# Kernel tuning notes

Measured on AMD Instinct MI355X. Metric: run time of the kernel, lower is better.

Reference implementation:

```python
import jax, jax.numpy as jnp
import numpy as np

TEMPERATURE = 0.07
HARD_K = 10
N, D, NUM_CLASSES = 8192, 256, 128


def setup_inputs() -> dict:
    key = jax.random.key(0)
    kf, kl = jax.random.split(key)
    feats = jax.random.normal(kf, (N, D), dtype=jnp.float32)
    labels = jax.random.randint(kl, (N,), 0, NUM_CLASSES, dtype=jnp.int64)
    return {"feats": feats, "labels": labels}


def _loss(feats, labels):
    n = feats.shape[0]
    # F.normalize(dim=-1) with eps=1e-12
    norm = jnp.maximum(jnp.linalg.norm(feats, axis=-1, keepdims=True), 1e-12)
    z = feats / norm
    sim = (z @ z.T) / TEMPERATURE  # [N, N]

    same = labels[:, None] == labels[None, :]
    eye = jnp.eye(n, dtype=bool)
    same_ns = same & ~eye          # same label, excluding self
    diff = ~same                   # different label

    neg_inf = jnp.float32(-jnp.inf)
    # uniform random positive per row via Gumbel-max over the same-label mask
    g = jax.random.gumbel(jax.random.key(42), (n, n), dtype=jnp.float32)
    pos_idx = jnp.argmax(jnp.where(same_ns, g, neg_inf), axis=1)  # [N]
    pos_logit = jnp.take_along_axis(sim, pos_idx[:, None], axis=1)[:, 0]

    # hard negatives: top-k of sims over different-label columns
    neg_sims = jnp.where(diff, sim, neg_inf)
    hard_vals, _ = jax.lax.top_k(neg_sims, HARD_K)  # [N, K]; exp(-inf)=0 handles rows with <K negatives

    num = jnp.exp(pos_logit)
    den = num + jnp.sum(jnp.exp(hard_vals), axis=1)
    li = -jnp.log(jnp.maximum(num / jnp.maximum(den, 1e-8), 1e-8))

    valid = jnp.any(same_ns, axis=1) & jnp.any(diff, axis=1)
    cnt = jnp.maximum(jnp.sum(valid), 1)
    return jnp.sum(jnp.where(valid, li, 0.0)) / cnt.astype(li.dtype)


def reference(feats, labels):
    return _loss(feats, labels)
```

## Files before the change

kernel.cpp:

```cpp
#include <hip/hip_runtime.h>
#include <cstdint>
#include <math.h>

#define N_     8192
#define D_     256
#define NLBL   128
#define TEMP_INV 14.285714285714286f
#define HARDK  10
#define THETA  0.16f
#define GCAP   256

#define RB     256
#define NCHUNK 32
#define CHUNK  (N_ / NCHUNK)
#define TILES  (CHUNK / 32)
#define CSLOT  16

typedef __attribute__((ext_vector_type(8)))  short bf16x8;
typedef __attribute__((ext_vector_type(16))) float f32x16;

__device__ __forceinline__ uint32_t rotl32(uint32_t x, int n) {
  return (x << n) | (x >> (32 - n));
}
__device__ uint32_t tf_bits(uint32_t idx) {
  uint32_t x0 = 0u, x1 = idx;
  const uint32_t k0 = 0u, k1 = 42u;
  const uint32_t k2 = k0 ^ k1 ^ 0x1BD11BDAu;
  x0 += k0; x1 += k1;
#define TFR(r) { x0 += x1; x1 = rotl32(x1, r); x1 ^= x0; }
  TFR(13) TFR(15) TFR(26) TFR(6)
  x0 += k1; x1 += k2 + 1u;
  TFR(17) TFR(29) TFR(16) TFR(24)
  x0 += k2; x1 += k0 + 2u;
  TFR(13) TFR(15) TFR(26) TFR(6)
  x0 += k0; x1 += k1 + 3u;
  TFR(17) TFR(29) TFR(16) TFR(24)
  x0 += k1; x1 += k2 + 4u;
  TFR(13) TFR(15) TFR(26) TFR(6)
  x0 += k2; x1 += k0 + 5u;
#undef TFR
  return x0 ^ x1;
}

__device__ __forceinline__ unsigned short f2bf(float x) {
  uint32_t b = __float_as_uint(x);
  return (unsigned short)((b + 0x7FFFu + ((b >> 16) & 1u)) >> 16);
}

__global__ __launch_bounds__(256) void prep_kernel(const float* __restrict__ feats,
                                                   float* __restrict__ inv_norm,
                                                   unsigned short* __restrict__ zbf) {
  const int i = blockIdx.x * 4 + (threadIdx.x >> 6);
  const int l = threadIdx.x & 63;
  float4 v = ((const float4*)feats)[(size_t)i * 64 + l];
  float ss = v.x * v.x + v.y * v.y + v.z * v.z + v.w * v.w;
#pragma unroll
  for (int o = 32; o; o >>= 1) ss += __shfl_xor(ss, o);
  float inv = 1.0f / fmaxf(sqrtf(ss), 1e-12f);
  if (l == 0) inv_norm[i] = inv;
  uint2 p;
  p.x = (uint32_t)f2bf(v.x * inv) | ((uint32_t)f2bf(v.y * inv) << 16);
  p.y = (uint32_t)f2bf(v.z * inv) | ((uint32_t)f2bf(v.w * inv) << 16);
  ((uint2*)zbf)[(size_t)i * 64 + l] = p;
}

__global__ __launch_bounds__(256) void transpose_kernel(const unsigned short* __restrict__ zbf,
                                                        unsigned short* __restrict__ zt) {
  __shared__ uint4 tile[64][33];
  const int tid = threadIdx.x;
  const int row0 = blockIdx.x * 64;
#pragma unroll
  for (int it = 0; it < 8; ++it) {
    int idx = it * 256 + tid;
    int r = idx >> 5, c = idx & 31;
    tile[r][c] = ((const uint4*)zbf)[(size_t)(row0 + r) * 32 + c];
  }
  __syncthreads();
#pragma unroll
  for (int it = 0; it < 8; ++it) {
    int c = it * 4 + (tid >> 6);
    int r = tid & 63;
    ((uint4*)zt)[(size_t)c * N_ + row0 + r] = tile[r][c];
  }
}

__global__ __launch_bounds__(256) void group_kernel(const int* __restrict__ labels,
                                                    uint32_t* __restrict__ mask_g,
                                                    int* __restrict__ glist,
                                                    int* __restrict__ cnt_g) {
  const int b = blockIdx.x;
  const int tid = threadIdx.x, lane = tid & 63, wv = tid >> 6;
  __shared__ int lcnt;
  if (tid == 0) lcnt = 0;
  __syncthreads();
  for (int it = 0; it < N_; it += 256) {
    int col = it + tid;
    bool pred = (labels[col] == b);
    unsigned long long m = __ballot(pred);
    if (lane == 0) {
      int w0 = (it + wv * 64) >> 5;
      mask_g[b * 256 + w0]     = (uint32_t)m;
      mask_g[b * 256 + w0 + 1] = (uint32_t)(m >> 32);
    }
    if (pred) {
      int p = atomicAdd(&lcnt, 1);
      if (p < GCAP) glist[b * GCAP + p] = col;
    }
  }
  __syncthreads();
  if (tid == 0) cnt_g[b] = lcnt;
}

__device__ __forceinline__ void stage_tile(const unsigned short* zt, char (*AbK)[1024],
                                           int colT, int wid, int l, int kg) {
  const char* base = (const char*)zt + ((size_t)kg * N_ + colT + (l & 31)) * 16;
#pragma unroll
  for (int q = 0; q < 4; ++q) {
    const int kk = wid * 4 + q;
    __builtin_amdgcn_global_load_lds(
        (const __attribute__((address_space(1))) void*)(base + (size_t)kk * (2 * N_ * 16)),
        (__attribute__((address_space(3))) void*)(&AbK[kk][0]), 16, 0, 0);
  }
}

#define INS8(H0,H1,H2,H3,H4,H5,H6,H7,POS,C) \
  { H0 = (POS==0)?(C):H0; H1 = (POS==1)?(C):H1; H2 = (POS==2)?(C):H2; H3 = (POS==3)?(C):H3; \
    H4 = (POS==4)?(C):H4; H5 = (POS==5)?(C):H5; H6 = (POS==6)?(C):H6; H7 = (POS==7)?(C):H7; \
    ++POS; }

__global__ __launch_bounds__(256, 2) void collect_kernel(const unsigned short* __restrict__ zt,
                                                         const int* __restrict__ labels,
                                                         const uint32_t* __restrict__ mask_g,
                                                         float* __restrict__ vals,
                                                         int* __restrict__ counts) {
  __shared__ char Ab[3][16][1024];

  const int tid = threadIdx.x;
  const int l = tid & 63, wid = tid >> 6;
  const int kg = l >> 5;
  const int bx = blockIdx.x;
  const int rc = bx & 31, cc = bx >> 5;
  const int row0 = rc * RB;
  const int col0 = cc * CHUNK;
  const int rowA = row0 + wid * 64 + (l & 31);
  const int rowB = rowA + 32;
  const int labA = labels[rowA];
  const int labB = labels[rowB];

  uint32_t mA[TILES], mB[TILES];
  {
    const uint4* ma = (const uint4*)(mask_g + labA * 256 + (col0 >> 5));
    const uint4* mb = (const uint4*)(mask_g + labB * 256 + (col0 >> 5));
    uint4 a0 = ma[0], a1 = ma[1], b0 = mb[0], b1 = mb[1];
    mA[0]=a0.x; mA[1]=a0.y; mA[2]=a0.z; mA[3]=a0.w;
    mA[4]=a1.x; mA[5]=a1.y; mA[6]=a1.z; mA[7]=a1.w;
    mB[0]=b0.x; mB[1]=b0.y; mB[2]=b0.z; mB[3]=b0.w;
    mB[4]=b1.x; mB[5]=b1.y; mB[6]=b1.z; mB[7]=b1.w;
  }

  bf16x8 bfA[16], bfB[16];
  {
    const uint4* ztq = (const uint4*)zt;
#pragma unroll
    for (int kk = 0; kk < 16; ++kk) {
      bfA[kk] = *(const bf16x8*)&ztq[(size_t)(kk * 2 + kg) * N_ + rowA];
      bfB[kk] = *(const bf16x8*)&ztq[(size_t)(kk * 2 + kg) * N_ + rowB];
    }
  }

  float hA0=0,hA1=0,hA2=0,hA3=0,hA4=0,hA5=0,hA6=0,hA7=0;
  float hB0=0,hB1=0,hB2=0,hB3=0,hB4=0,hB5=0,hB6=0,hB7=0;
  int posA = 0, posB = 0;

  stage_tile(zt, Ab[0], col0 + 0 * 32, wid, l, kg);
  stage_tile(zt, Ab[1], col0 + 1 * 32, wid, l, kg);
  asm volatile("s_waitcnt vmcnt(4)" ::: "memory");
  __builtin_amdgcn_s_barrier();
  __builtin_amdgcn_sched_barrier(0);

#pragma unroll
  for (int t = 0; t < TILES; ++t) {
    if (t + 2 < TILES) stage_tile(zt, Ab[(t + 2) % 3], col0 + (t + 2) * 32, wid, l, kg);

    const uint32_t wshA = mA[t] >> (kg * 4);
    const uint32_t wshB = mB[t] >> (kg * 4);

    f32x16 accA, accB;
#pragma unroll
    for (int r = 0; r < 16; ++r) { accA[r] = 0.f; accB[r] = 0.f; }
    __builtin_amdgcn_s_setprio(1);
#pragma unroll
    for (int kk = 0; kk < 16; ++kk) {
      bf16x8 a = *(const bf16x8*)&Ab[t % 3][kk][l * 16];
      accA = __builtin_amdgcn_mfma_f32_32x32x16_bf16(a, bfA[kk], accA, 0, 0, 0);
      accB = __builtin_amdgcn_mfma_f32_32x32x16_bf16(a, bfB[kk], accB, 0, 0, 0);
    }
    __builtin_amdgcn_s_setprio(0);

#pragma unroll
    for (int r = 0; r < 16; ++r) {
      const int cpos = (r & 3) + 8 * (r >> 2);
      float cA = accA[r];
      if ((((wshA >> cpos) & 1u) == 0u) && (cA > THETA)) {
        INS8(hA0,hA1,hA2,hA3,hA4,hA5,hA6,hA7, posA, cA);
      }
      float cB = accB[r];
      if ((((wshB >> cpos) & 1u) == 0u) && (cB > THETA)) {
        INS8(hB0,hB1,hB2,hB3,hB4,hB5,hB6,hB7, posB, cB);
      }
    }

    if (t < TILES - 2) {
      asm volatile("s_waitcnt vmcnt(4)" ::: "memory");
      __builtin_amdgcn_s_barrier();
      __builtin_amdgcn_sched_barrier(0);
    } else if (t == TILES - 2) {
      asm volatile("s_waitcnt vmcnt(0)" ::: "memory");
      __builtin_amdgcn_s_barrier();
      __builtin_amdgcn_sched_barrier(0);
    }
  }

  {
    float4 a0 = {hA0, hA1, hA2, hA3};
    float4 a1 = {hA4, hA5, hA6, hA7};
    float4 b0 = {hB0, hB1, hB2, hB3};
    float4 b1 = {hB4, hB5, hB6, hB7};
    float* dA = vals + ((size_t)rowA * NCHUNK + cc) * CSLOT + kg * 8;
    float* dB = vals + ((size_t)rowB * NCHUNK + cc) * CSLOT + kg * 8;
    *(float4*)(dA)     = a0;
    *(float4*)(dA + 4) = a1;
    *(float4*)(dB)     = b0;
    *(float4*)(dB + 4) = b1;
    counts[(rowA * NCHUNK + cc) * 2 + kg] = posA;
    counts[(rowB * NCHUNK + cc) * 2 + kg] = posB;
  }
}

__global__ __launch_bounds__(256) void finalize_kernel(
    const float* __restrict__ feats, const int* __restrict__ labels,
    const float* __restrict__ inv_norm,
    const int* __restrict__ glist, const int* __restrict__ cnt_g,
    const int* __restrict__ counts, const float* __restrict__ vals,
    float* __restrict__ li, int* __restrict__ valid) {
  const int row = blockIdx.x * 4 + (threadIdx.x >> 6);
  const int lane = threadIdx.x & 63;
  const int lab = labels[row];
  const int gc = cnt_g[lab];
  const int gn = gc < GCAP ? gc : GCAP;
  const float4* feats4 = (const float4*)feats;

  uint32_t bk = 0u; int bj = -1;
  for (int e = lane; e < gn; e += 64) {
    int j = glist[lab * GCAP + e];
    if (j != row) {
      uint32_t key = tf_bits((uint32_t)row * (uint32_t)N_ + (uint32_t)j) >> 9;
      if (bj < 0 || key > bk || (key == bk && j < bj)) { bk = key; bj = j; }
    }
  }
#pragma unroll
  for (int o = 32; o; o >>= 1) {
    uint32_t ok = __shfl_xor(bk, o);
    int oj = __shfl_xor(bj, o);
    if (oj >= 0 && (bj < 0 || ok > bk || (ok == bk && oj < bj))) { bk = ok; bj = oj; }
  }

  float pc = 0.f;
  if (bj >= 0) {
    float4 a = feats4[(size_t)row * 64 + lane];
    float4 b = feats4[(size_t)bj * 64 + lane];
    float p = a.x * b.x + a.y * b.y + a.z * b.z + a.w * b.w;
#pragma unroll
    for (int o = 32; o; o >>= 1) p += __shfl_xor(p, o);
    pc = p * inv_norm[row] * inv_norm[bj];
  }

  float vv[8];
  int ovf = 0;
#pragma unroll
  for (int q = 0; q < 8; ++q) {
    int s = lane + 64 * q;
    int cell = s >> 4, wi = s & 15;
    int c0 = counts[(row * NCHUNK + cell) * 2 + 0];
    int c1 = counts[(row * NCHUNK + cell) * 2 + 1];
    ovf |= ((c0 > 8) || (c1 > 8)) ? 1 : 0;
    float val = vals[(size_t)row * (NCHUNK * CSLOT) + s];
    bool live = (wi < 8) ? (wi < c0) : ((wi - 8) < c1);
    vv[q] = live ? val : -INFINITY;
  }

  float num = expf(pc * TEMP_INV);
  float den = num;
  int got = 0;
#pragma unroll 1
  for (int it = 0; it < HARDK; ++it) {
    float lm = fmaxf(fmaxf(fmaxf(vv[0], vv[1]), fmaxf(vv[2], vv[3])),
                     fmaxf(fmaxf(vv[4], vv[5]), fmaxf(vv[6], vv[7])));
    float wm = lm;
#pragma unroll
    for (int o = 32; o; o >>= 1) wm = fmaxf(wm, __shfl_xor(wm, o));
    if (wm < -1e37f) break;
    den += expf(wm * TEMP_INV);
    ++got;
    unsigned long long b = __ballot(lm == wm);
    int fl = __ffsll((long long)b) - 1;
    if (lane == fl) {
      if      (vv[0] == wm) vv[0] = -INFINITY;
      else if (vv[1] == wm) vv[1] = -INFINITY;
      else if (vv[2] == wm) vv[2] = -INFINITY;
      else if (vv[3] == wm) vv[3] = -INFINITY;
      else if (vv[4] == wm) vv[4] = -INFINITY;
      else if (vv[5] == wm) vv[5] = -INFINITY;
      else if (vv[6] == wm) vv[6] = -INFINITY;
      else                  vv[7] = -INFINITY;
    }
  }

  const int ndiff = N_ - gc;
  const bool vld = (bj >= 0) && (ndiff > 0);
  const int want = ndiff < HARDK ? ndiff : HARDK;

  if (vld && (__any(ovf) || got < want)) {
    float tk[HARDK];
#pragma unroll
    for (int k = 0; k < HARDK; ++k) tk[k] = -INFINITY;
    const float invr = inv_norm[row];
    const float4 a = feats4[(size_t)row * 64 + lane];
#pragma unroll 1
    for (int j = 0; j < N_; ++j) {
      if (j == row || labels[j] == lab) continue;
      float4 b = feats4[(size_t)j * 64 + lane];
      float p = a.x * b.x + a.y * b.y + a.z * b.z + a.w * b.w;
#pragma unroll
      for (int o = 32; o; o >>= 1) p += __shfl_xor(p, o);
      float c = p * invr * inv_norm[j];
      if (c > tk[0]) {
        tk[0] = c;
#pragma unroll
        for (int q = 0; q < HARDK - 1; ++q)
          if (tk[q] > tk[q + 1]) { float tmp = tk[q]; tk[q] = tk[q + 1]; tk[q + 1] = tmp; }
      }
    }
    den = num;
#pragma unroll
    for (int k = 0; k < HARDK; ++k)
      if (tk[k] > -1e37f) den += expf(tk[k] * TEMP_INV);
  }

  float L = 0.f;
  if (vld) L = -logf(fmaxf(num / fmaxf(den, 1e-8f), 1e-8f));
  if (lane == 0) {
    li[row] = L;
    valid[row] = vld ? 1 : 0;
  }
}

__global__ __launch_bounds__(256) void reduce_kernel(const float* __restrict__ li,
                                                     const int* __restrict__ valid,
                                                     float* __restrict__ out) {
  __shared__ float ssum[4];
  __shared__ int scnt[4];
  float s = 0.f; int c = 0;
  for (int i = threadIdx.x; i < N_; i += 256) { s += li[i]; c += valid[i]; }
#pragma unroll
  for (int o = 32; o; o >>= 1) { s += __shfl_down(s, o); c += __shfl_down(c, o); }
  if ((threadIdx.x & 63) == 0) { ssum[threadIdx.x >> 6] = s; scnt[threadIdx.x >> 6] = c; }
  __syncthreads();
  if (threadIdx.x == 0) {
    float S = 0.f; int C = 0;
    for (int w = 0; w < 4; ++w) { S += ssum[w]; C += scnt[w]; }
    out[0] = S / (float)(C > 0 ? C : 1);
  }
}

extern "C" void kernel_launch(void* const* d_in, const int* in_sizes, int n_in,
                              void* d_out, int out_size, void* d_ws, size_t ws_size,
                              hipStream_t stream) {
  const float* feats  = (const float*)d_in[0];
  const int*   labels = (const int*)d_in[1];
  float* out = (float*)d_out;

  char* w = (char*)d_ws;
  unsigned short* zbf = (unsigned short*)w;  w += (size_t)N_ * D_ * 2;
  unsigned short* zt  = (unsigned short*)w;  w += (size_t)N_ * D_ * 2;
  float* inv_norm = (float*)w;               w += (size_t)N_ * 4;
  uint32_t* mask_g = (uint32_t*)w;           w += (size_t)NLBL * 256 * 4;
  int* glist = (int*)w;                      w += (size_t)NLBL * GCAP * 4;
  int* cnt_g = (int*)w;                      w += (size_t)NLBL * 4;
  int* counts = (int*)w;                     w += (size_t)N_ * NCHUNK * 2 * 4;
  float* vals = (float*)w;                   w += (size_t)N_ * NCHUNK * CSLOT * 4;
  float* li_arr = (float*)w;                 w += (size_t)N_ * 4;
  int* valid_arr = (int*)w;                  w += (size_t)N_ * 4;

  hipLaunchKernelGGL(prep_kernel, dim3(N_ / 4), dim3(256), 0, stream, feats, inv_norm, zbf);
  hipLaunchKernelGGL(transpose_kernel, dim3(N_ / 64), dim3(256), 0, stream, zbf, zt);
  hipLaunchKernelGGL(group_kernel, dim3(NLBL), dim3(256), 0, stream, labels, mask_g, glist, cnt_g);
  hipLaunchKernelGGL(collect_kernel, dim3(32 * NCHUNK), dim3(256), 0, stream,
                     zt, labels, mask_g, vals, counts);
  hipLaunchKernelGGL(finalize_kernel, dim3(N_ / 4), dim3(256), 0, stream,
                     feats, labels, inv_norm, glist, cnt_g, counts, vals, li_arr, valid_arr);
  hipLaunchKernelGGL(reduce_kernel, dim3(1), dim3(256), 0, stream, li_arr, valid_arr, out);
}
```

Measured before the change: 101.6 us.

## Load column tiles directly from global memory instead of LDS triple-buffering

Removes the shared-memory triple-buffered staging of column tiles (global_load_lds plus barriers) and has each wave read its B operand fragments straight from global memory. The mask words are now read per tile from global rather than preloaded into registers. This drops the LDS footprint and all block-level barriers, but each of the four waves now fetches the same column tile independently. That relies on L1/L2 caching, and global-load latency is exposed right before the MFMAs with no explicit prefetch.

```diff
diff --git a/kernel.cpp b/kernel.cpp
--- a/kernel.cpp
+++ b/kernel.cpp
@@ -111,17 +111,6 @@
   if (tid == 0) cnt_g[b] = lcnt;
 }
 
-__device__ __forceinline__ void stage_tile(const unsigned short* zt, char (*AbK)[1024],
-                                           int colT, int wid, int l, int kg) {
-  const char* base = (const char*)zt + ((size_t)kg * N_ + colT + (l & 31)) * 16;
-#pragma unroll
-  for (int q = 0; q < 4; ++q) {
-    const int kk = wid * 4 + q;
-    __builtin_amdgcn_global_load_lds(
-        (const __attribute__((address_space(1))) void*)(base + (size_t)kk * (2 * N_ * 16)),
-        (__attribute__((address_space(3))) void*)(&AbK[kk][0]), 16, 0, 0);
-  }
-}
 
 #define INS8(H0,H1,H2,H3,H4,H5,H6,H7,POS,C) \
   { H0 = (POS==0)?(C):H0; H1 = (POS==1)?(C):H1; H2 = (POS==2)?(C):H2; H3 = (POS==3)?(C):H3; \
@@ -133,8 +122,6 @@
                                                          const uint32_t* __restrict__ mask_g,
                                                          float* __restrict__ vals,
                                                          int* __restrict__ counts) {
-  __shared__ char Ab[3][16][1024];
-
   const int tid = threadIdx.x;
   const int l = tid & 63, wid = tid >> 6;
   const int kg = l >> 5;
@@ -146,44 +133,28 @@
   const int rowB = rowA + 32;
   const int labA = labels[rowA];
   const int labB = labels[rowB];
-
-  uint32_t mA[TILES], mB[TILES];
-  {
-    const uint4* ma = (const uint4*)(mask_g + labA * 256 + (col0 >> 5));
-    const uint4* mb = (const uint4*)(mask_g + labB * 256 + (col0 >> 5));
-    uint4 a0 = ma[0], a1 = ma[1], b0 = mb[0], b1 = mb[1];
-    mA[0]=a0.x; mA[1]=a0.y; mA[2]=a0.z; mA[3]=a0.w;
-    mA[4]=a1.x; mA[5]=a1.y; mA[6]=a1.z; mA[7]=a1.w;
-    mB[0]=b0.x; mB[1]=b0.y; mB[2]=b0.z; mB[3]=b0.w;
-    mB[4]=b1.x; mB[5]=b1.y; mB[6]=b1.z; mB[7]=b1.w;
-  }
+  const uint32_t* mgA = mask_g + labA * 256 + (col0 >> 5);
+  const uint32_t* mgB = mask_g + labB * 256 + (col0 >> 5);
+
+  const uint4* ztq = (const uint4*)zt;
 
   bf16x8 bfA[16], bfB[16];
-  {
-    const uint4* ztq = (const uint4*)zt;
-#pragma unroll
-    for (int kk = 0; kk < 16; ++kk) {
-      bfA[kk] = *(const bf16x8*)&ztq[(size_t)(kk * 2 + kg) * N_ + rowA];
-      bfB[kk] = *(const bf16x8*)&ztq[(size_t)(kk * 2 + kg) * N_ + rowB];
-    }
+#pragma unroll
+  for (int kk = 0; kk < 16; ++kk) {
+    bfA[kk] = *(const bf16x8*)&ztq[(size_t)(kk * 2 + kg) * N_ + rowA];
+    bfB[kk] = *(const bf16x8*)&ztq[(size_t)(kk * 2 + kg) * N_ + rowB];
   }
 
   float hA0=0,hA1=0,hA2=0,hA3=0,hA4=0,hA5=0,hA6=0,hA7=0;
   float hB0=0,hB1=0,hB2=0,hB3=0,hB4=0,hB5=0,hB6=0,hB7=0;
   int posA = 0, posB = 0;
 
-  stage_tile(zt, Ab[0], col0 + 0 * 32, wid, l, kg);
-  stage_tile(zt, Ab[1], col0 + 1 * 32, wid, l, kg);
-  asm volatile("s_waitcnt vmcnt(4)" ::: "memory");
-  __builtin_amdgcn_s_barrier();
-  __builtin_amdgcn_sched_barrier(0);
+  const uint4* abase = ztq + (size_t)kg * N_ + col0 + (l & 31);
 
 #pragma unroll
   for (int t = 0; t < TILES; ++t) {
-    if (t + 2 < TILES) stage_tile(zt, Ab[(t + 2) % 3], col0 + (t + 2) * 32, wid, l, kg);
-
-    const uint32_t wshA = mA[t] >> (kg * 4);
-    const uint32_t wshB = mB[t] >> (kg * 4);
+    const uint32_t wshA = mgA[t] >> (kg * 4);
+    const uint32_t wshB = mgB[t] >> (kg * 4);
 
     f32x16 accA, accB;
 #pragma unroll
@@ -191,7 +162,7 @@
     __builtin_amdgcn_s_setprio(1);
 #pragma unroll
     for (int kk = 0; kk < 16; ++kk) {
-      bf16x8 a = *(const bf16x8*)&Ab[t % 3][kk][l * 16];
+      bf16x8 a = *(const bf16x8*)&abase[(size_t)kk * (2 * N_) + t * 32];
       accA = __builtin_amdgcn_mfma_f32_32x32x16_bf16(a, bfA[kk], accA, 0, 0, 0);
       accB = __builtin_amdgcn_mfma_f32_32x32x16_bf16(a, bfB[kk], accB, 0, 0, 0);
     }
@@ -208,16 +179,6 @@
       if ((((wshB >> cpos) & 1u) == 0u) && (cB > THETA)) {
         INS8(hB0,hB1,hB2,hB3,hB4,hB5,hB6,hB7, posB, cB);
       }
-    }
-
-    if (t < TILES - 2) {
-      asm volatile("s_waitcnt vmcnt(4)" ::: "memory");
-      __builtin_amdgcn_s_barrier();
-      __builtin_amdgcn_sched_barrier(0);
-    } else if (t == TILES - 2) {
-      asm volatile("s_waitcnt vmcnt(0)" ::: "memory");
-      __builtin_amdgcn_s_barrier();
-      __builtin_amdgcn_sched_barrier(0);
     }
   }
 
```

New measurement: 118.0 us. 1.16x slower.

## Fuse prep, transpose and grouping kernels; fold final reduction into finalize

Applied to the files above, without the earlier changes.

Merges normalization, bf16 conversion and transpose into one kernel that stages rows in shared memory, so the zbf round trip through global memory goes away. The label grouping runs on extra blocks of the same launch. The separate reduce kernel is replaced by fixed-point 64-bit atomics plus a last-block-done counter inside finalize. Together this cuts the kernel launch count from six to three. The trade-offs are lower parallelism in prep, since it now uses only 128 blocks, and fixed-point accumulation that assumes every loss value is non-negative and small.

```diff
diff --git a/kernel.cpp b/kernel.cpp
--- a/kernel.cpp
+++ b/kernel.cpp
@@ -42,73 +42,69 @@
   return x0 ^ x1;
 }
 
-__device__ __forceinline__ unsigned short f2bf(float x) {
+__device__ __forceinline__ uint32_t f2bf(float x) {
   uint32_t b = __float_as_uint(x);
-  return (unsigned short)((b + 0x7FFFu + ((b >> 16) & 1u)) >> 16);
-}
-
-__global__ __launch_bounds__(256) void prep_kernel(const float* __restrict__ feats,
-                                                   float* __restrict__ inv_norm,
-                                                   unsigned short* __restrict__ zbf) {
-  const int i = blockIdx.x * 4 + (threadIdx.x >> 6);
-  const int l = threadIdx.x & 63;
-  float4 v = ((const float4*)feats)[(size_t)i * 64 + l];
-  float ss = v.x * v.x + v.y * v.y + v.z * v.z + v.w * v.w;
-#pragma unroll
-  for (int o = 32; o; o >>= 1) ss += __shfl_xor(ss, o);
-  float inv = 1.0f / fmaxf(sqrtf(ss), 1e-12f);
-  if (l == 0) inv_norm[i] = inv;
-  uint2 p;
-  p.x = (uint32_t)f2bf(v.x * inv) | ((uint32_t)f2bf(v.y * inv) << 16);
-  p.y = (uint32_t)f2bf(v.z * inv) | ((uint32_t)f2bf(v.w * inv) << 16);
-  ((uint2*)zbf)[(size_t)i * 64 + l] = p;
-}
-
-__global__ __launch_bounds__(256) void transpose_kernel(const unsigned short* __restrict__ zbf,
-                                                        unsigned short* __restrict__ zt) {
+  return (b + 0x7FFFu + ((b >> 16) & 1u)) >> 16;
+}
+
+__global__ __launch_bounds__(256) void prep_group_kernel(
+    const float* __restrict__ feats, const int* __restrict__ labels,
+    float* __restrict__ inv_norm, unsigned short* __restrict__ zt,
+    uint32_t* __restrict__ mask_g, int* __restrict__ glist, int* __restrict__ cnt_g,
+    unsigned long long* __restrict__ accum) {
   __shared__ uint4 tile[64][33];
+  __shared__ int lcnt;
   const int tid = threadIdx.x;
-  const int row0 = blockIdx.x * 64;
-#pragma unroll
-  for (int it = 0; it < 8; ++it) {
-    int idx = it * 256 + tid;
-    int r = idx >> 5, c = idx & 31;
-    tile[r][c] = ((const uint4*)zbf)[(size_t)(row0 + r) * 32 + c];
-  }
-  __syncthreads();
-#pragma unroll
-  for (int it = 0; it < 8; ++it) {
-    int c = it * 4 + (tid >> 6);
-    int r = tid & 63;
-    ((uint4*)zt)[(size_t)c * N_ + row0 + r] = tile[r][c];
-  }
-}
-
-__global__ __launch_bounds__(256) void group_kernel(const int* __restrict__ labels,
-                                                    uint32_t* __restrict__ mask_g,
-                                                    int* __restrict__ glist,
-                                                    int* __restrict__ cnt_g) {
-  const int b = blockIdx.x;
-  const int tid = threadIdx.x, lane = tid & 63, wv = tid >> 6;
-  __shared__ int lcnt;
-  if (tid == 0) lcnt = 0;
-  __syncthreads();
-  for (int it = 0; it < N_; it += 256) {
-    int col = it + tid;
-    bool pred = (labels[col] == b);
-    unsigned long long m = __ballot(pred);
-    if (lane == 0) {
-      int w0 = (it + wv * 64) >> 5;
-      mask_g[b * 256 + w0]     = (uint32_t)m;
-      mask_g[b * 256 + w0 + 1] = (uint32_t)(m >> 32);
-    }
-    if (pred) {
-      int p = atomicAdd(&lcnt, 1);
-      if (p < GCAP) glist[b * GCAP + p] = col;
-    }
-  }
-  __syncthreads();
-  if (tid == 0) cnt_g[b] = lcnt;
+
+  if (blockIdx.x == 0 && tid < 3) accum[tid] = 0ULL;
+
+  if (blockIdx.x < 128) {
+    const int row0 = blockIdx.x * 64;
+    const int wv = tid >> 6, l = tid & 63;
+#pragma unroll 4
+    for (int rr = 0; rr < 16; ++rr) {
+      const int rloc = wv * 16 + rr;
+      const int row = row0 + rloc;
+      float4 v = ((const float4*)feats)[(size_t)row * 64 + l];
+      float ss = v.x * v.x + v.y * v.y + v.z * v.z + v.w * v.w;
+#pragma unroll
+      for (int o = 32; o; o >>= 1) ss += __shfl_xor(ss, o);
+      float inv = 1.0f / fmaxf(sqrtf(ss), 1e-12f);
+      if (l == 0) inv_norm[row] = inv;
+      uint2 p;
+      p.x = f2bf(v.x * inv) | (f2bf(v.y * inv) << 16);
+      p.y = f2bf(v.z * inv) | (f2bf(v.w * inv) << 16);
+      *(uint2*)((char*)&tile[0][0] + rloc * 528 + l * 8) = p;
+    }
+    __syncthreads();
+#pragma unroll
+    for (int it = 0; it < 8; ++it) {
+      int c = it * 4 + (tid >> 6);
+      int r = tid & 63;
+      ((uint4*)zt)[(size_t)c * N_ + row0 + r] = tile[r][c];
+    }
+  } else {
+    const int b = blockIdx.x - 128;
+    const int lane = tid & 63, wv = tid >> 6;
+    if (tid == 0) lcnt = 0;
+    __syncthreads();
+    for (int it = 0; it < N_; it += 256) {
+      int col = it + tid;
+      bool pred = (labels[col] == b);
+      unsigned long long m = __ballot(pred);
+      if (lane == 0) {
+        int w0 = (it + wv * 64) >> 5;
+        mask_g[b * 256 + w0]     = (uint32_t)m;
+        mask_g[b * 256 + w0 + 1] = (uint32_t)(m >> 32);
+      }
+      if (pred) {
+        int p = atomicAdd(&lcnt, 1);
+        if (p < GCAP) glist[b * GCAP + p] = col;
+      }
+    }
+    __syncthreads();
+    if (tid == 0) cnt_g[b] = lcnt;
+  }
 }
 
 __device__ __forceinline__ void stage_tile(const unsigned short* zt, char (*AbK)[1024],
@@ -242,7 +238,9 @@
     const float* __restrict__ inv_norm,
     const int* __restrict__ glist, const int* __restrict__ cnt_g,
     const int* __restrict__ counts, const float* __restrict__ vals,
-    float* __restrict__ li, int* __restrict__ valid) {
+    unsigned long long* __restrict__ accum, float* __restrict__ out) {
+  __shared__ unsigned long long sfx[4];
+  __shared__ unsigned int scnt[4];
   const int row = blockIdx.x * 4 + (threadIdx.x >> 6);
   const int lane = threadIdx.x & 63;
   const int lab = labels[row];
@@ -349,27 +347,25 @@
 
   float L = 0.f;
   if (vld) L = -logf(fmaxf(num / fmaxf(den, 1e-8f), 1e-8f));
+
   if (lane == 0) {
-    li[row] = L;
-    valid[row] = vld ? 1 : 0;
-  }
-}
-
-__global__ __launch_bounds__(256) void reduce_kernel(const float* __restrict__ li,
-                                                     const int* __restrict__ valid,
-                                                     float* __restrict__ out) {
-  __shared__ float ssum[4];
-  __shared__ int scnt[4];
-  float s = 0.f; int c = 0;
-  for (int i = threadIdx.x; i < N_; i += 256) { s += li[i]; c += valid[i]; }
-#pragma unroll
-  for (int o = 32; o; o >>= 1) { s += __shfl_down(s, o); c += __shfl_down(c, o); }
-  if ((threadIdx.x & 63) == 0) { ssum[threadIdx.x >> 6] = s; scnt[threadIdx.x >> 6] = c; }
+    sfx[threadIdx.x >> 6]  = (unsigned long long)((double)L * 4294967296.0);
+    scnt[threadIdx.x >> 6] = vld ? 1u : 0u;
+  }
   __syncthreads();
   if (threadIdx.x == 0) {
-    float S = 0.f; int C = 0;
-    for (int w = 0; w < 4; ++w) { S += ssum[w]; C += scnt[w]; }
-    out[0] = S / (float)(C > 0 ? C : 1);
+    unsigned long long S = sfx[0] + sfx[1] + sfx[2] + sfx[3];
+    unsigned int C = scnt[0] + scnt[1] + scnt[2] + scnt[3];
+    atomicAdd(&accum[0], S);
+    atomicAdd((unsigned int*)&accum[1], C);
+    __threadfence();
+    unsigned int old = atomicAdd((unsigned int*)&accum[2], 1u);
+    if (old == gridDim.x - 1) {
+      unsigned long long FS = atomicAdd(&accum[0], 0ULL);
+      unsigned int FC = atomicAdd((unsigned int*)&accum[1], 0u);
+      double s = (double)FS * (1.0 / 4294967296.0);
+      out[0] = (float)(s / (double)(FC > 0u ? FC : 1u));
+    }
   }
 }
 
@@ -381,23 +377,19 @@
   float* out = (float*)d_out;
 
   char* w = (char*)d_ws;
-  unsigned short* zbf = (unsigned short*)w;  w += (size_t)N_ * D_ * 2;
   unsigned short* zt  = (unsigned short*)w;  w += (size_t)N_ * D_ * 2;
   float* inv_norm = (float*)w;               w += (size_t)N_ * 4;
   uint32_t* mask_g = (uint32_t*)w;           w += (size_t)NLBL * 256 * 4;
   int* glist = (int*)w;                      w += (size_t)NLBL * GCAP * 4;
   int* cnt_g = (int*)w;                      w += (size_t)NLBL * 4;
+  unsigned long long* accum = (unsigned long long*)w;  w += 64;
   int* counts = (int*)w;                     w += (size_t)N_ * NCHUNK * 2 * 4;
   float* vals = (float*)w;                   w += (size_t)N_ * NCHUNK * CSLOT * 4;
-  float* li_arr = (float*)w;                 w += (size_t)N_ * 4;
-  int* valid_arr = (int*)w;                  w += (size_t)N_ * 4;
-
-  hipLaunchKernelGGL(prep_kernel, dim3(N_ / 4), dim3(256), 0, stream, feats, inv_norm, zbf);
-  hipLaunchKernelGGL(transpose_kernel, dim3(N_ / 64), dim3(256), 0, stream, zbf, zt);
-  hipLaunchKernelGGL(group_kernel, dim3(NLBL), dim3(256), 0, stream, labels, mask_g, glist, cnt_g);
+
+  hipLaunchKernelGGL(prep_group_kernel, dim3(256), dim3(256), 0, stream,
+                     feats, labels, inv_norm, zt, mask_g, glist, cnt_g, accum);
   hipLaunchKernelGGL(collect_kernel, dim3(32 * NCHUNK), dim3(256), 0, stream,
                      zt, labels, mask_g, vals, counts);
   hipLaunchKernelGGL(finalize_kernel, dim3(N_ / 4), dim3(256), 0, stream,
-                     feats, labels, inv_norm, glist, cnt_g, counts, vals, li_arr, valid_arr);
-  hipLaunchKernelGGL(reduce_kernel, dim3(1), dim3(256), 0, stream, li_arr, valid_arr, out);
-}
+                     feats, labels, inv_norm, glist, cnt_g, counts, vals, accum, out);
+}
```

New measurement: 149.7 us. 1.47x slower.
